# Kernel tuning notes

Measured on AMD Instinct MI355X. Metric: run time of the kernel, lower is better.

Reference implementation:

```python
import jax, jax.numpy as jnp
import numpy as np

NH = 16  # num_heads from init_kwargs


def setup_inputs() -> dict:
    key = jax.random.key(0)
    ks = jax.random.split(key, 7)
    B, L, S, H = 4, 2, 1024, 1024
    s = 0.02  # weight init scale to keep logits numerically tame
    return {
        "x": jax.random.normal(ks[0], (B, S, H), jnp.float32),
        "y": jax.random.normal(ks[1], (L, B, S, H), jnp.float32),
        "bias": jax.random.normal(ks[2], (B, 1, 1, S), jnp.float32),
        "Wq": jax.random.normal(ks[3], (H, H), jnp.float32) * s,
        "Wk": jax.random.normal(ks[4], (L, H, H), jnp.float32) * s,
        "Wv": jax.random.normal(ks[5], (L, H, H), jnp.float32) * s,
        "Wo": jax.random.normal(ks[6], (H, H), jnp.float32) * s,
    }


def reference(x, y, bias, Wq, Wk, Wv, Wo):
    # x: [B, Lq, H]; y: [L, B, Lk, H] (stacked list of per-link memories)
    B, Lq, H = x.shape
    L, _, Lk, _ = y.shape
    d = H // NH

    # shared query projection, split heads: [B, NH, Lq, d], pre-scaled
    q = (x @ Wq).reshape(B, Lq, NH, d).transpose(0, 2, 1, 3) * (d ** -0.5)

    # per-link K/V projections, split heads -> [B, L, NH, Lk, d]
    kp = jnp.einsum('lbsh,lhe->lbse', y, Wk).reshape(L, B, Lk, NH, d).transpose(1, 0, 3, 2, 4)
    vp = jnp.einsum('lbsh,lhe->lbse', y, Wv).reshape(L, B, Lk, NH, d).transpose(1, 0, 3, 2, 4)

    # per-link logits [B, L, NH, Lq, Lk] + broadcast bias (concat across links == broadcast)
    logits = jnp.einsum('bhqd,blhkd->blhqk', q, kp) + bias[:, None]

    # computation_mode == 1: joint softmax over the link-summed logits
    joint = logits.sum(axis=1)                # [B, NH, Lq, Lk]
    w = jax.nn.softmax(joint, axis=-1)        # (training=False -> no dropout)

    # sum_l (w @ v_l) == w @ sum_l v_l  (w is shared across links)
    ctx = jnp.einsum('bhqk,bhkd->bhqd', w, vp.sum(axis=1))

    # combine heads [B, Lq, H] and output projection
    out = ctx.transpose(0, 2, 1, 3).reshape(B, Lq, H) @ Wo
    return out
```

## Files before the change

kernel.cpp:

```cpp
#include <hip/hip_runtime.h>
#include <cstdint>

typedef __bf16 bf16_t;
typedef bf16_t bf16x4 __attribute__((ext_vector_type(4)));
typedef bf16_t bf16x8 __attribute__((ext_vector_type(8)));
typedef float f32x4 __attribute__((ext_vector_type(4)));
typedef float f32x16 __attribute__((ext_vector_type(16)));

#define GLD_LDS16(g, l)                                                        \
  __builtin_amdgcn_global_load_lds(                                            \
      (const __attribute__((address_space(1))) void*)(g),                      \
      (__attribute__((address_space(3))) void*)(l), 16, 0, 0)

#define LOG2E 1.44269504088896340736f

static __device__ __forceinline__ unsigned short bf16_bits(float f) {
  bf16_t h = (bf16_t)f;
  return __builtin_bit_cast(unsigned short, h);
}

__global__ void prep_kernel(const float* __restrict__ x,
                            const float* __restrict__ y,
                            const float* __restrict__ Wq,
                            const float* __restrict__ Wk,
                            const float* __restrict__ Wv,
                            const float* __restrict__ Wo,
                            bf16_t* __restrict__ xb, bf16_t* __restrict__ yb,
                            bf16_t* __restrict__ WqT,
                            bf16_t* __restrict__ WkvT,
                            bf16_t* __restrict__ WoT) {
  __shared__ float tile[32][33];
  int bid = blockIdx.x;
  if (bid < 6144) {
    int i = bid * 256 + threadIdx.x;
    const float* src;
    bf16_t* dst;
    if (i < 524288) { src = x; dst = xb; }
    else            { src = y; dst = yb; i -= 524288; }
    const float4* s = (const float4*)src;
    float4 a = s[i * 2];
    float4 b = s[i * 2 + 1];
    bf16x8 o;
    o[0] = (bf16_t)a.x; o[1] = (bf16_t)a.y; o[2] = (bf16_t)a.z; o[3] = (bf16_t)a.w;
    o[4] = (bf16_t)b.x; o[5] = (bf16_t)b.y; o[6] = (bf16_t)b.z; o[7] = (bf16_t)b.w;
    *(bf16x8*)(dst + (size_t)i * 8) = o;
    return;
  }
  bid -= 6144;
  const float* src; bf16_t* dst; int R, lb;
  if (bid < 1024)      { src = Wq; dst = WqT;                        R = 1024; lb = bid; }
  else if (bid < 3072) { src = Wk; dst = WkvT;                       R = 2048; lb = bid - 1024; }
  else if (bid < 5120) { src = Wv; dst = WkvT + (size_t)1024 * 2048; R = 2048; lb = bid - 3072; }
  else                 { src = Wo; dst = WoT;                        R = 1024; lb = bid - 5120; }
  int c0 = (lb & 31) << 5, r0 = (lb >> 5) << 5;
  int tc = threadIdx.x & 31, tr = threadIdx.x >> 5;
#pragma unroll
  for (int i = 0; i < 4; i++)
    tile[tr + i * 8][tc] = src[(size_t)(r0 + tr + i * 8) * 1024 + c0 + tc];
  __syncthreads();
#pragma unroll
  for (int i = 0; i < 4; i++)
    dst[(size_t)(c0 + tr + i * 8) * R + r0 + tc] = (bf16_t)tile[tc][tr + i * 8];
}

#define GEMM_STAGE(buf, kt)                                                    \
  {                                                                            \
    const int kbase = (kt) * 32;                                               \
    int kg0 = kbase + ak0;                                                     \
    const bf16_t* s0 = (kg0 < Ksplit)                                          \
                           ? (A0 + (size_t)(m0 + ar0) * 1024 + kg0)            \
                           : (A1 + (size_t)(m0 + ar0) * 1024 + (kg0 - Ksplit));\
    GLD_LDS16(s0, As[buf] + c0 * 8);                                           \
    int kg1 = kbase + ak1;                                                     \
    const bf16_t* s1 = (kg1 < Ksplit)                                          \
                           ? (A0 + (size_t)(m0 + ar1) * 1024 + kg1)            \
                           : (A1 + (size_t)(m0 + ar1) * 1024 + (kg1 - Ksplit));\
    GLD_LDS16(s1, As[buf] + c1 * 8);                                           \
    const bf16_t* b0 = BT + (size_t)(n0 + ar0) * Ktot + kbase + ak0;           \
    GLD_LDS16(b0, Bs[buf] + c0 * 8);                                           \
    const bf16_t* b1 = BT + (size_t)(n0 + ar1) * Ktot + kbase + ak1;           \
    GLD_LDS16(b1, Bs[buf] + c1 * 8);                                           \
  }

#define GEMM_DECLS                                                             \
  const int t = threadIdx.x, w = t >> 6, l = t & 63;                           \
  const int l15 = l & 15, l4 = l >> 4;                                         \
  const int wr = w >> 1, wc = w & 1;                                           \
  const int c0 = t, c1 = t + 256;                                              \
  const int ar0 = c0 >> 2, ar1 = c1 >> 2;                                      \
  const int ak0 = ((c0 & 3) ^ ((ar0 >> 1) & 3)) * 8;                           \
  const int ak1 = ((c1 & 3) ^ ((ar1 >> 1) & 3)) * 8;                           \
  int offA[4], offB[4];                                                        \
  _Pragma("unroll") for (int mi = 0; mi < 4; mi++) {                           \
    int rA = wr * 64 + mi * 16 + l15;                                          \
    offA[mi] = rA * 32 + (l4 ^ ((rA >> 1) & 3)) * 8;                           \
    int rB = wc * 64 + mi * 16 + l15;                                          \
    offB[mi] = rB * 32 + (l4 ^ ((rB >> 1) & 3)) * 8;                           \
  }

#define GEMM_MAINLOOP                                                          \
  GEMM_STAGE(0, 0);                                                            \
  __syncthreads();                                                             \
  int cur = 0;                                                                 \
  for (int kt = 0; kt < nkt; ++kt) {                                           \
    if (kt + 1 < nkt) GEMM_STAGE(cur ^ 1, kt + 1);                             \
    bf16x8 af[4], bfr[4];                                                      \
    _Pragma("unroll") for (int mi = 0; mi < 4; mi++)                           \
        af[mi] = *(const bf16x8*)&As[cur][offA[mi]];                           \
    _Pragma("unroll") for (int ni = 0; ni < 4; ni++)                           \
        bfr[ni] = *(const bf16x8*)&Bs[cur][offB[ni]];                          \
    _Pragma("unroll") for (int mi = 0; mi < 4; mi++)                           \
        _Pragma("unroll") for (int ni = 0; ni < 4; ni++)                       \
            acc[mi][ni] = __builtin_amdgcn_mfma_f32_16x16x32_bf16(             \
                af[mi], bfr[ni], acc[mi][ni], 0, 0, 0);                        \
    __syncthreads();                                                           \
    cur ^= 1;                                                                  \
  }

__global__ __launch_bounds__(256, 2) void qkv_kernel(
    const bf16_t* __restrict__ xbp, const bf16_t* __restrict__ ybp,
    const bf16_t* __restrict__ WqT, const bf16_t* __restrict__ WkvT,
    bf16_t* __restrict__ Qb, bf16_t* __restrict__ Kb,
    bf16_t* __restrict__ VTb) {
  __shared__ bf16_t As[2][128 * 32];
  __shared__ bf16_t Bs[2][128 * 32];
  GEMM_DECLS
  const bool isQ = blockIdx.x < 256;
  const int i = isQ ? blockIdx.x : blockIdx.x - 256;
  const int ybt = (i & 7) * 4 + ((i >> 3) & 3);
  const int xbt = i >> 5;
  const int m0 = ybt * 128, n0 = xbt * 128;
  const bf16_t* A0 = isQ ? xbp : ybp;
  const bf16_t* A1 = isQ ? xbp : ybp + (size_t)4096 * 1024;
  const int Ksplit = 1024;
  const bf16_t* BT = isQ ? WqT : WkvT;
  const int Ktot = isQ ? 1024 : 2048;
  const int nkt = Ktot >> 5;
  f32x4 acc[4][4] = {};

  GEMM_MAINLOOP

#pragma unroll
  for (int mi = 0; mi < 4; mi++) {
#pragma unroll
    for (int ni = 0; ni < 4; ni++) {
      const int rbase = m0 + wr * 64 + mi * 16 + l4 * 4;
      const int col = n0 + wc * 64 + ni * 16 + l15;
      if (isQ) {
#pragma unroll
        for (int rr = 0; rr < 4; rr++)
          Qb[(size_t)(rbase + rr) * 1024 + col] =
              (bf16_t)(acc[mi][ni][rr] * (0.125f * LOG2E));
      } else if (n0 < 1024) {
#pragma unroll
        for (int rr = 0; rr < 4; rr++)
          Kb[(size_t)(rbase + rr) * 1024 + col] = (bf16_t)acc[mi][ni][rr];
      } else {
        union { unsigned short u[4]; uint2 v; } pk;
#pragma unroll
        for (int rr = 0; rr < 4; rr++)
          pk.u[rr] = bf16_bits(acc[mi][ni][rr]);
        *(uint2*)&VTb[(size_t)(col - 1024) * 4096 + rbase] = pk.v;
      }
    }
  }
}

__global__ __launch_bounds__(256, 2) void gemm_o(const bf16_t* __restrict__ A0,
                                                 const bf16_t* __restrict__ BT,
                                                 float* __restrict__ Cp) {
  __shared__ bf16_t As[2][128 * 32];
  __shared__ bf16_t Bs[2][128 * 32];
  GEMM_DECLS
  const int i = blockIdx.x;
  const int ybt = (i & 7) * 4 + ((i >> 3) & 3);
  const int xbt = i >> 5;
  const int m0 = ybt * 128, n0 = xbt * 128;
  const bf16_t* A1 = A0;
  const int Ksplit = 1024, Ktot = 1024, nkt = 32;
  f32x4 acc[4][4] = {};

  GEMM_MAINLOOP

#pragma unroll
  for (int mi = 0; mi < 4; mi++) {
#pragma unroll
    for (int ni = 0; ni < 4; ni++) {
      const int rbase = m0 + wr * 64 + mi * 16 + l4 * 4;
      const int col = n0 + wc * 64 + ni * 16 + l15;
#pragma unroll
      for (int rr = 0; rr < 4; rr++)
        Cp[(size_t)(rbase + rr) * 1024 + col] = acc[mi][ni][rr];
    }
  }
}

__global__ __launch_bounds__(256, 2) void attn_kernel(
    const bf16_t* __restrict__ Q, const bf16_t* __restrict__ K,
    const bf16_t* __restrict__ VT, const float* __restrict__ bias,
    bf16_t* __restrict__ ctx) {
  __shared__ bf16_t Ks[2][64 * 64];
  __shared__ bf16_t Vs[2][64 * 64];
  const int t = threadIdx.x, w = t >> 6, l = t & 63;
  const int l31 = l & 31, hi = l >> 5;
  const int id = blockIdx.x;
  const int bh = id & 63, qt = id >> 6;
  const int b = bh >> 4, h = bh & 15;
  const int q_local = w * 32 + l31;

  bf16x8 qf[4];
  {
    const bf16_t* Qp =
        Q + (size_t)(b * 1024 + qt * 128 + q_local) * 1024 + h * 64 + hi * 8;
#pragma unroll
    for (int ds = 0; ds < 4; ds++) qf[ds] = *(const bf16x8*)&Qp[ds * 16];
  }

#define ATTN_STAGE(buf, kt)                                                    \
  {                                                                            \
    _Pragma("unroll") for (int j = 0; j < 2; j++) {                            \
      int c = t + j * 256;                                                     \
      int row = c >> 3, sl = (c & 7) ^ (row & 7);                              \
      const bf16_t* srck =                                                     \
          K + (size_t)(b * 1024 + (kt) * 64 + row) * 1024 + h * 64 + sl * 8;   \
      GLD_LDS16(srck, Ks[buf] + c * 8);                                        \
      const bf16_t* srcv =                                                     \
          VT + (size_t)(h * 64 + row) * 4096 + b * 1024 + (kt) * 64 + sl * 8;  \
      GLD_LDS16(srcv, Vs[buf] + c * 8);                                        \
    }                                                                          \
  }

  float mrun = -INFINITY, lrun = 0.f;
  f32x16 cacc[2] = {};

  ATTN_STAGE(0, 0);
  __syncthreads();
  int cur = 0;
  for (int kt = 0; kt < 16; ++kt) {
    if (kt + 1 < 16) ATTN_STAGE(cur ^ 1, kt + 1);

    f32x16 sacc[2] = {};
#pragma unroll
    for (int ds = 0; ds < 4; ds++) {
#pragma unroll
      for (int kg = 0; kg < 2; kg++) {
        int krow = kg * 32 + l31;
        int eoff = (krow * 64 + ds * 16 + hi * 8) ^ ((krow & 7) << 3);
        bf16x8 kf = *(const bf16x8*)&Ks[cur][eoff];
        sacc[kg] = __builtin_amdgcn_mfma_f32_32x32x16_bf16(kf, qf[ds],
                                                           sacc[kg], 0, 0, 0);
      }
    }
#pragma unroll
    for (int kg = 0; kg < 2; kg++) {
#pragma unroll
      for (int mm = 0; mm < 4; mm++) {
        f32x4 bb = *(const f32x4*)&bias[b * 1024 + kt * 64 + kg * 32 + mm * 8 +
                                        hi * 4];
#pragma unroll
        for (int rr = 0; rr < 4; rr++)
          sacc[kg][mm * 4 + rr] += (2.0f * LOG2E) * bb[rr];
      }
    }
    float tm = -INFINITY;
#pragma unroll
    for (int kg = 0; kg < 2; kg++)
#pragma unroll
      for (int r = 0; r < 16; r++) tm = fmaxf(tm, sacc[kg][r]);
    tm = fmaxf(tm, __shfl_xor(tm, 32));
    float mnew = fmaxf(mrun, tm);
    float sc = exp2f(mrun - mnew);
    float rsum = 0.f;
#pragma unroll
    for (int kg = 0; kg < 2; kg++)
#pragma unroll
      for (int r = 0; r < 16; r++) {
        float p = exp2f(sacc[kg][r] - mnew);
        sacc[kg][r] = p;
        rsum += p;
      }
    rsum += __shfl_xor(rsum, 32);
    lrun = lrun * sc + rsum;
    mrun = mnew;
#pragma unroll
    for (int dg = 0; dg < 2; dg++)
#pragma unroll
      for (int r = 0; r < 16; r++) cacc[dg][r] *= sc;

    bf16x8 pb[4];
#pragma unroll
    for (int kg = 0; kg < 2; kg++) {
#pragma unroll
      for (int tt = 0; tt < 2; tt++) {
        uint32_t w0A, w1A, w0B, w1B;
        const int mA = 2 * tt, mB = 2 * tt + 1;
        asm("v_cvt_pk_bf16_f32 %0, %1, %2"
            : "=v"(w0A)
            : "v"(sacc[kg][4 * mA + 0]), "v"(sacc[kg][4 * mA + 1]));
        asm("v_cvt_pk_bf16_f32 %0, %1, %2"
            : "=v"(w1A)
            : "v"(sacc[kg][4 * mA + 2]), "v"(sacc[kg][4 * mA + 3]));
        asm("v_cvt_pk_bf16_f32 %0, %1, %2"
            : "=v"(w0B)
            : "v"(sacc[kg][4 * mB + 0]), "v"(sacc[kg][4 * mB + 1]));
        asm("v_cvt_pk_bf16_f32 %0, %1, %2"
            : "=v"(w1B)
            : "v"(sacc[kg][4 * mB + 2]), "v"(sacc[kg][4 * mB + 3]));
        asm("v_permlane32_swap_b32 %0, %1" : "+v"(w0A), "+v"(w0B));
        asm("v_permlane32_swap_b32 %0, %1" : "+v"(w1A), "+v"(w1B));
        union { uint32_t u[4]; bf16x8 v; } pk;
        pk.u[0] = w0A; pk.u[1] = w1A; pk.u[2] = w0B; pk.u[3] = w1B;
        pb[kg * 2 + tt] = pk.v;
      }
    }
#pragma unroll
    for (int dg = 0; dg < 2; dg++) {
#pragma unroll
      for (int k4 = 0; k4 < 4; k4++) {
        int vrow = dg * 32 + l31;
        int eoff = (vrow * 64 + k4 * 16 + hi * 8) ^ ((vrow & 7) << 3);
        bf16x8 vf = *(const bf16x8*)&Vs[cur][eoff];
        cacc[dg] = __builtin_amdgcn_mfma_f32_32x32x16_bf16(vf, pb[k4],
                                                           cacc[dg], 0, 0, 0);
      }
    }
    __syncthreads();
    cur ^= 1;
  }

  bf16_t* T = (bf16_t*)Ks;
  {
    float inv = 1.0f / lrun;
#pragma unroll
    for (int dg = 0; dg < 2; dg++) {
#pragma unroll
      for (int m = 0; m < 4; m++) {
        bf16x4 tv;
#pragma unroll
        for (int rr = 0; rr < 4; rr++)
          tv[rr] = (bf16_t)(cacc[dg][4 * m + rr] * inv);
        int d0 = dg * 32 + m * 8 + hi * 4;
        *(bf16x4*)&T[q_local * 64 + (d0 ^ ((q_local & 7) << 3))] = tv;
      }
    }
  }
  __syncthreads();
#pragma unroll
  for (int c = t; c < 1024; c += 256) {
    int row = c >> 3, col8 = c & 7;
    bf16x8 v = *(const bf16x8*)&T[row * 64 + ((col8 * 8) ^ ((row & 7) << 3))];
    *(bf16x8*)&ctx[(size_t)(b * 1024 + qt * 128 + row) * 1024 + h * 64 +
                   col8 * 8] = v;
  }
#undef ATTN_STAGE
}

extern "C" void kernel_launch(void* const* d_in, const int* in_sizes, int n_in,
                              void* d_out, int out_size, void* d_ws,
                              size_t ws_size, hipStream_t stream) {
  const float* x = (const float*)d_in[0];
  const float* y = (const float*)d_in[1];
  const float* bias = (const float*)d_in[2];
  const float* Wq = (const float*)d_in[3];
  const float* Wk = (const float*)d_in[4];
  const float* Wv = (const float*)d_in[5];
  const float* Wo = (const float*)d_in[6];
  float* out = (float*)d_out;

  char* ws = (char*)d_ws;
  const size_t MB = 1024 * 1024;
  bf16_t* xb   = (bf16_t*)(ws + 0 * MB);
  bf16_t* yb   = (bf16_t*)(ws + 8 * MB);
  bf16_t* WqT  = (bf16_t*)(ws + 24 * MB);
  bf16_t* WkvT = (bf16_t*)(ws + 26 * MB);
  bf16_t* WoT  = (bf16_t*)(ws + 34 * MB);
  bf16_t* Qb   = (bf16_t*)(ws + 36 * MB);
  bf16_t* Kb   = (bf16_t*)(ws + 44 * MB);
  bf16_t* VTb  = (bf16_t*)(ws + 52 * MB);
  bf16_t* ctxb = (bf16_t*)(ws + 60 * MB);

  prep_kernel<<<12288, 256, 0, stream>>>(x, y, Wq, Wk, Wv, Wo, xb, yb, WqT,
                                         WkvT, WoT);
  qkv_kernel<<<768, 256, 0, stream>>>(xb, yb, WqT, WkvT, Qb, Kb, VTb);
  attn_kernel<<<512, 256, 0, stream>>>(Qb, Kb, VTb, bias, ctxb);
  gemm_o<<<256, 256, 0, stream>>>(ctxb, WoT, out);
}
```

Before: 141.6 us.

## Double attention K/V stage depth and narrow output GEMM tiles for more blocks

The attention kernel now loads 128-key chunks of K and V into shared memory per stage and processes them in two 64-key halves. This halves the number of barriers and loop iterations, at the cost of doubled LDS footprint, and uses a new V swizzle for the 128-wide rows. The output projection GEMM switches from 128x128 to 128x64 tiles with its own inline main loop and launches 512 blocks instead of 256 to improve CU occupancy and parallelism. The narrower tiles re-read the A operand more often.

```diff
diff --git a/kernel.cpp b/kernel.cpp
--- a/kernel.cpp
+++ b/kernel.cpp
@@ -170,24 +170,73 @@
                                                  const bf16_t* __restrict__ BT,
                                                  float* __restrict__ Cp) {
   __shared__ bf16_t As[2][128 * 32];
-  __shared__ bf16_t Bs[2][128 * 32];
-  GEMM_DECLS
+  __shared__ bf16_t Bs[2][64 * 32];
+  const int t = threadIdx.x, w = t >> 6, l = t & 63;
+  const int l15 = l & 15, l4 = l >> 4;
+  const int wr = w >> 1, wc = w & 1;
+  const int c0 = t, c1 = t + 256, c2 = t;
+  const int ar0 = c0 >> 2, ar1 = c1 >> 2, br2 = c2 >> 2;
+  const int ak0 = ((c0 & 3) ^ ((ar0 >> 1) & 3)) * 8;
+  const int ak1 = ((c1 & 3) ^ ((ar1 >> 1) & 3)) * 8;
+  const int bk2 = ((c2 & 3) ^ ((br2 >> 1) & 3)) * 8;
+  int offA[4], offB[2];
+#pragma unroll
+  for (int mi = 0; mi < 4; mi++) {
+    int rA = wr * 64 + mi * 16 + l15;
+    offA[mi] = rA * 32 + (l4 ^ ((rA >> 1) & 3)) * 8;
+  }
+#pragma unroll
+  for (int ni = 0; ni < 2; ni++) {
+    int rB = wc * 32 + ni * 16 + l15;
+    offB[ni] = rB * 32 + (l4 ^ ((rB >> 1) & 3)) * 8;
+  }
   const int i = blockIdx.x;
   const int ybt = (i & 7) * 4 + ((i >> 3) & 3);
   const int xbt = i >> 5;
-  const int m0 = ybt * 128, n0 = xbt * 128;
-  const bf16_t* A1 = A0;
-  const int Ksplit = 1024, Ktot = 1024, nkt = 32;
-  f32x4 acc[4][4] = {};
-
-  GEMM_MAINLOOP
+  const int m0 = ybt * 128, n0 = xbt * 64;
+  const int nkt = 32;
+  f32x4 acc[4][2] = {};
+
+#define OST(buf, kt)                                                           \
+  {                                                                            \
+    const int kbase = (kt) * 32;                                               \
+    const bf16_t* s0 = A0 + (size_t)(m0 + ar0) * 1024 + kbase + ak0;           \
+    GLD_LDS16(s0, As[buf] + c0 * 8);                                           \
+    const bf16_t* s1 = A0 + (size_t)(m0 + ar1) * 1024 + kbase + ak1;           \
+    GLD_LDS16(s1, As[buf] + c1 * 8);                                           \
+    const bf16_t* b0 = BT + (size_t)(n0 + br2) * 1024 + kbase + bk2;           \
+    GLD_LDS16(b0, Bs[buf] + c2 * 8);                                           \
+  }
+
+  OST(0, 0);
+  __syncthreads();
+  int cur = 0;
+  for (int kt = 0; kt < nkt; ++kt) {
+    if (kt + 1 < nkt) OST(cur ^ 1, kt + 1);
+    bf16x8 af[4], bfr[2];
+#pragma unroll
+    for (int mi = 0; mi < 4; mi++)
+      af[mi] = *(const bf16x8*)&As[cur][offA[mi]];
+#pragma unroll
+    for (int ni = 0; ni < 2; ni++)
+      bfr[ni] = *(const bf16x8*)&Bs[cur][offB[ni]];
+#pragma unroll
+    for (int mi = 0; mi < 4; mi++)
+#pragma unroll
+      for (int ni = 0; ni < 2; ni++)
+        acc[mi][ni] = __builtin_amdgcn_mfma_f32_16x16x32_bf16(
+            af[mi], bfr[ni], acc[mi][ni], 0, 0, 0);
+    __syncthreads();
+    cur ^= 1;
+  }
+#undef OST
 
 #pragma unroll
   for (int mi = 0; mi < 4; mi++) {
 #pragma unroll
-    for (int ni = 0; ni < 4; ni++) {
+    for (int ni = 0; ni < 2; ni++) {
       const int rbase = m0 + wr * 64 + mi * 16 + l4 * 4;
-      const int col = n0 + wc * 64 + ni * 16 + l15;
+      const int col = n0 + wc * 32 + ni * 16 + l15;
 #pragma unroll
       for (int rr = 0; rr < 4; rr++)
         Cp[(size_t)(rbase + rr) * 1024 + col] = acc[mi][ni][rr];
@@ -199,8 +248,8 @@
     const bf16_t* __restrict__ Q, const bf16_t* __restrict__ K,
     const bf16_t* __restrict__ VT, const float* __restrict__ bias,
     bf16_t* __restrict__ ctx) {
-  __shared__ bf16_t Ks[2][64 * 64];
-  __shared__ bf16_t Vs[2][64 * 64];
+  __shared__ bf16_t Ks[2][128 * 64];
+  __shared__ bf16_t Vs[2][64 * 128];
   const int t = threadIdx.x, w = t >> 6, l = t & 63;
   const int l31 = l & 31, hi = l >> 5;
   const int id = blockIdx.x;
@@ -218,14 +267,16 @@
 
 #define ATTN_STAGE(buf, kt)                                                    \
   {                                                                            \
-    _Pragma("unroll") for (int j = 0; j < 2; j++) {                            \
+    _Pragma("unroll") for (int j = 0; j < 4; j++) {                            \
       int c = t + j * 256;                                                     \
-      int row = c >> 3, sl = (c & 7) ^ (row & 7);                              \
+      int rowk = c >> 3, slk = (c & 7) ^ (rowk & 7);                           \
       const bf16_t* srck =                                                     \
-          K + (size_t)(b * 1024 + (kt) * 64 + row) * 1024 + h * 64 + sl * 8;   \
+          K + (size_t)(b * 1024 + (kt) * 128 + rowk) * 1024 + h * 64 + slk * 8;\
       GLD_LDS16(srck, Ks[buf] + c * 8);                                        \
+      int rowv = c >> 4, slv = (c & 15) ^ ((rowv & 7) << 1);                   \
       const bf16_t* srcv =                                                     \
-          VT + (size_t)(h * 64 + row) * 4096 + b * 1024 + (kt) * 64 + sl * 8;  \
+          VT + (size_t)(h * 64 + rowv) * 4096 + b * 1024 + (kt) * 128 +        \
+          slv * 8;                                                             \
       GLD_LDS16(srcv, Vs[buf] + c * 8);                                        \
     }                                                                          \
   }
@@ -236,92 +287,96 @@
   ATTN_STAGE(0, 0);
   __syncthreads();
   int cur = 0;
-  for (int kt = 0; kt < 16; ++kt) {
-    if (kt + 1 < 16) ATTN_STAGE(cur ^ 1, kt + 1);
-
-    f32x16 sacc[2] = {};
-#pragma unroll
-    for (int ds = 0; ds < 4; ds++) {
+  for (int kts = 0; kts < 8; ++kts) {
+    if (kts + 1 < 8) ATTN_STAGE(cur ^ 1, kts + 1);
+
+#pragma unroll
+    for (int half = 0; half < 2; ++half) {
+      f32x16 sacc[2] = {};
+#pragma unroll
+      for (int ds = 0; ds < 4; ds++) {
+#pragma unroll
+        for (int kg = 0; kg < 2; kg++) {
+          int krow = half * 64 + kg * 32 + l31;
+          int eoff = krow * 64 + (((ds * 2 + hi) ^ (krow & 7)) * 8);
+          bf16x8 kf = *(const bf16x8*)&Ks[cur][eoff];
+          sacc[kg] = __builtin_amdgcn_mfma_f32_32x32x16_bf16(
+              kf, qf[ds], sacc[kg], 0, 0, 0);
+        }
+      }
 #pragma unroll
       for (int kg = 0; kg < 2; kg++) {
-        int krow = kg * 32 + l31;
-        int eoff = (krow * 64 + ds * 16 + hi * 8) ^ ((krow & 7) << 3);
-        bf16x8 kf = *(const bf16x8*)&Ks[cur][eoff];
-        sacc[kg] = __builtin_amdgcn_mfma_f32_32x32x16_bf16(kf, qf[ds],
-                                                           sacc[kg], 0, 0, 0);
-      }
-    }
-#pragma unroll
-    for (int kg = 0; kg < 2; kg++) {
-#pragma unroll
-      for (int mm = 0; mm < 4; mm++) {
-        f32x4 bb = *(const f32x4*)&bias[b * 1024 + kt * 64 + kg * 32 + mm * 8 +
-                                        hi * 4];
-#pragma unroll
-        for (int rr = 0; rr < 4; rr++)
-          sacc[kg][mm * 4 + rr] += (2.0f * LOG2E) * bb[rr];
-      }
-    }
-    float tm = -INFINITY;
-#pragma unroll
-    for (int kg = 0; kg < 2; kg++)
-#pragma unroll
-      for (int r = 0; r < 16; r++) tm = fmaxf(tm, sacc[kg][r]);
-    tm = fmaxf(tm, __shfl_xor(tm, 32));
-    float mnew = fmaxf(mrun, tm);
-    float sc = exp2f(mrun - mnew);
-    float rsum = 0.f;
-#pragma unroll
-    for (int kg = 0; kg < 2; kg++)
-#pragma unroll
-      for (int r = 0; r < 16; r++) {
-        float p = exp2f(sacc[kg][r] - mnew);
-        sacc[kg][r] = p;
-        rsum += p;
-      }
-    rsum += __shfl_xor(rsum, 32);
-    lrun = lrun * sc + rsum;
-    mrun = mnew;
-#pragma unroll
-    for (int dg = 0; dg < 2; dg++)
-#pragma unroll
-      for (int r = 0; r < 16; r++) cacc[dg][r] *= sc;
-
-    bf16x8 pb[4];
-#pragma unroll
-    for (int kg = 0; kg < 2; kg++) {
-#pragma unroll
-      for (int tt = 0; tt < 2; tt++) {
-        uint32_t w0A, w1A, w0B, w1B;
-        const int mA = 2 * tt, mB = 2 * tt + 1;
-        asm("v_cvt_pk_bf16_f32 %0, %1, %2"
-            : "=v"(w0A)
-            : "v"(sacc[kg][4 * mA + 0]), "v"(sacc[kg][4 * mA + 1]));
-        asm("v_cvt_pk_bf16_f32 %0, %1, %2"
-            : "=v"(w1A)
-            : "v"(sacc[kg][4 * mA + 2]), "v"(sacc[kg][4 * mA + 3]));
-        asm("v_cvt_pk_bf16_f32 %0, %1, %2"
-            : "=v"(w0B)
-            : "v"(sacc[kg][4 * mB + 0]), "v"(sacc[kg][4 * mB + 1]));
-        asm("v_cvt_pk_bf16_f32 %0, %1, %2"
-            : "=v"(w1B)
-            : "v"(sacc[kg][4 * mB + 2]), "v"(sacc[kg][4 * mB + 3]));
-        asm("v_permlane32_swap_b32 %0, %1" : "+v"(w0A), "+v"(w0B));
-        asm("v_permlane32_swap_b32 %0, %1" : "+v"(w1A), "+v"(w1B));
-        union { uint32_t u[4]; bf16x8 v; } pk;
-        pk.u[0] = w0A; pk.u[1] = w1A; pk.u[2] = w0B; pk.u[3] = w1B;
-        pb[kg * 2 + tt] = pk.v;
-      }
-    }
-#pragma unroll
-    for (int dg = 0; dg < 2; dg++) {
-#pragma unroll
-      for (int k4 = 0; k4 < 4; k4++) {
-        int vrow = dg * 32 + l31;
-        int eoff = (vrow * 64 + k4 * 16 + hi * 8) ^ ((vrow & 7) << 3);
-        bf16x8 vf = *(const bf16x8*)&Vs[cur][eoff];
-        cacc[dg] = __builtin_amdgcn_mfma_f32_32x32x16_bf16(vf, pb[k4],
-                                                           cacc[dg], 0, 0, 0);
+#pragma unroll
+        for (int mm = 0; mm < 4; mm++) {
+          f32x4 bb = *(const f32x4*)&bias[b * 1024 + kts * 128 + half * 64 +
+                                          kg * 32 + mm * 8 + hi * 4];
+#pragma unroll
+          for (int rr = 0; rr < 4; rr++)
+            sacc[kg][mm * 4 + rr] += (2.0f * LOG2E) * bb[rr];
+        }
+      }
+      float tm = -INFINITY;
+#pragma unroll
+      for (int kg = 0; kg < 2; kg++)
+#pragma unroll
+        for (int r = 0; r < 16; r++) tm = fmaxf(tm, sacc[kg][r]);
+      tm = fmaxf(tm, __shfl_xor(tm, 32));
+      float mnew = fmaxf(mrun, tm);
+      float sc = exp2f(mrun - mnew);
+      float rsum = 0.f;
+#pragma unroll
+      for (int kg = 0; kg < 2; kg++)
+#pragma unroll
+        for (int r = 0; r < 16; r++) {
+          float p = exp2f(sacc[kg][r] - mnew);
+          sacc[kg][r] = p;
+          rsum += p;
+        }
+      rsum += __shfl_xor(rsum, 32);
+      lrun = lrun * sc + rsum;
+      mrun = mnew;
+#pragma unroll
+      for (int dg = 0; dg < 2; dg++)
+#pragma unroll
+        for (int r = 0; r < 16; r++) cacc[dg][r] *= sc;
+
+      bf16x8 pb[4];
+#pragma unroll
+      for (int kg = 0; kg < 2; kg++) {
+#pragma unroll
+        for (int tt = 0; tt < 2; tt++) {
+          uint32_t w0A, w1A, w0B, w1B;
+          const int mA = 2 * tt, mB = 2 * tt + 1;
+          asm("v_cvt_pk_bf16_f32 %0, %1, %2"
+              : "=v"(w0A)
+              : "v"(sacc[kg][4 * mA + 0]), "v"(sacc[kg][4 * mA + 1]));
+          asm("v_cvt_pk_bf16_f32 %0, %1, %2"
+              : "=v"(w1A)
+              : "v"(sacc[kg][4 * mA + 2]), "v"(sacc[kg][4 * mA + 3]));
+          asm("v_cvt_pk_bf16_f32 %0, %1, %2"
+              : "=v"(w0B)
+              : "v"(sacc[kg][4 * mB + 0]), "v"(sacc[kg][4 * mB + 1]));
+          asm("v_cvt_pk_bf16_f32 %0, %1, %2"
+              : "=v"(w1B)
+              : "v"(sacc[kg][4 * mB + 2]), "v"(sacc[kg][4 * mB + 3]));
+          asm("v_permlane32_swap_b32 %0, %1" : "+v"(w0A), "+v"(w0B));
+          asm("v_permlane32_swap_b32 %0, %1" : "+v"(w1A), "+v"(w1B));
+          union { uint32_t u[4]; bf16x8 v; } pk;
+          pk.u[0] = w0A; pk.u[1] = w1A; pk.u[2] = w0B; pk.u[3] = w1B;
+          pb[kg * 2 + tt] = pk.v;
+        }
+      }
+#pragma unroll
+      for (int dg = 0; dg < 2; dg++) {
+#pragma unroll
+        for (int k4 = 0; k4 < 4; k4++) {
+          int vrow = dg * 32 + l31;
+          int s = half * 8 + k4 * 2 + hi;
+          int eoff = vrow * 128 + ((s ^ ((vrow & 7) << 1)) * 8);
+          bf16x8 vf = *(const bf16x8*)&Vs[cur][eoff];
+          cacc[dg] = __builtin_amdgcn_mfma_f32_32x32x16_bf16(
+              vf, pb[k4], cacc[dg], 0, 0, 0);
+        }
       }
     }
     __syncthreads();
@@ -383,5 +438,5 @@
                                          WkvT, WoT);
   qkv_kernel<<<768, 256, 0, stream>>>(xb, yb, WqT, WkvT, Qb, Kb, VTb);
   attn_kernel<<<512, 256, 0, stream>>>(Qb, Kb, VTb, bias, ctxb);
-  gemm_o<<<256, 256, 0, stream>>>(ctxb, WoT, out);
-}
+  gemm_o<<<512, 256, 0, stream>>>(ctxb, WoT, out);
+}
```

Measured after the change: 134.3 us. -5.2%, faster.
